# Kernel tuning notes

Hardware: AMD Instinct MI355X
Metric: run time of the kernel (lower is better)

The kernel has to match this reference:

```python
import math
import jax, jax.numpy as jnp
import numpy as np

B, S, D = 2, 2048, 4096
H = 32
HD = D // H  # 128
CLIP_QKV = 8.0
ALIBI_BIAS_MAX = 8
LN_EPS = 1e-5


def _get_alibi_slopes(total_num_heads: int, alibi_bias_max: int) -> np.ndarray:
    next_pow2 = 2 ** math.ceil(math.log2(total_num_heads))
    m = np.arange(1, next_pow2 + 1, dtype=np.float32) * (alibi_bias_max / next_pow2)
    slopes = 1.0 / np.power(2.0, m)
    if next_pow2 != total_num_heads:
        slopes = np.concatenate([slopes[1::2], slopes[::2]])[:total_num_heads]
    return slopes


ALIBI_SLOPES = jnp.asarray(_get_alibi_slopes(H, ALIBI_BIAS_MAX))  # [H]


def _layernorm(x, w, b):
    mu = jnp.mean(x, axis=-1, keepdims=True)
    var = jnp.mean(jnp.square(x - mu), axis=-1, keepdims=True)
    return (x - mu) * jax.lax.rsqrt(var + LN_EPS) * w + b


def setup_inputs() -> dict:
    key = jax.random.key(0)
    ks = jax.random.split(key, 3)
    scale_in = 1.0 / math.sqrt(D)
    return {
        "hidden_states": jax.random.normal(ks[0], (B, S, D), jnp.float32),
        "Wqkv": jax.random.normal(ks[1], (D, 3 * D), jnp.float32) * scale_in,
        "Wout": jax.random.normal(ks[2], (D, D), jnp.float32) * scale_in,
        "q_ln_w": jnp.ones((D,), jnp.float32),
        "q_ln_b": jnp.zeros((D,), jnp.float32),
        "k_ln_w": jnp.ones((D,), jnp.float32),
        "k_ln_b": jnp.zeros((D,), jnp.float32),
    }


def reference(hidden_states, Wqkv, Wout, q_ln_w, q_ln_b, k_ln_w, k_ln_b):
    # QKV projection + clamp
    qkv = jnp.clip(hidden_states @ Wqkv, -CLIP_QKV, CLIP_QKV)  # [B,S,3D]
    q, k, v = jnp.split(qkv, [D, 2 * D], axis=-1)
    # QK LayerNorm over full d_model (as in MPT qk_ln)
    q = _layernorm(q, q_ln_w, q_ln_b)
    k = _layernorm(k, k_ln_w, k_ln_b)
    # split heads
    q = q.reshape(B, S, H, HD)
    k = k.reshape(B, S, H, HD)
    v = v.reshape(B, S, H, HD)
    scale = HD ** (-0.5)
    scores = jnp.einsum("bqhd,bkhd->bhqk", q, k) * scale  # [B,H,S,S]
    # ALiBi bias: -slope * (i - j), causal mask j <= i
    pos = jnp.arange(S)
    dist = pos[:, None] - pos[None, :]  # [S,S], i - j
    bias = -ALIBI_SLOPES[:, None, None] * dist.astype(jnp.float32)  # [H,S,S]
    causal = dist >= 0
    scores = jnp.where(causal[None, None], scores + bias[None], -jnp.inf)
    attn = jax.nn.softmax(scores, axis=-1)
    out = jnp.einsum("bhqk,bkhd->bqhd", attn, v).reshape(B, S, D)
    return out @ Wout
```

## Files before the change

kernel.cpp:

```cpp
#include <hip/hip_runtime.h>
#include <hip/hip_bf16.h>
#include <stdint.h>

#define BB 2
#define SS 2048
#define DD 4096
#define HH 32
#define HDD 128

typedef unsigned short u16;
typedef unsigned int u32;

constexpr float CLIPV  = 8.0f;
constexpr float LN_EPS_ = 1e-5f;
constexpr float SCALE_ = 0.08838834764831845f;
constexpr float LOG2E_ = 1.4426950408889634f;

using f32x4 = __attribute__((ext_vector_type(4))) float;
using s16x8 = __attribute__((ext_vector_type(8))) short;

__device__ inline u16 f2bf(float f) {
  union { float f; u32 u; } v; v.f = f;
  u32 r = (v.u + 0x7FFFu + ((v.u >> 16) & 1u)) >> 16;
  return (u16)r;
}
__device__ inline float bf2f(u16 u) {
  union { u32 u; float f; } v; v.u = ((u32)u) << 16;
  return v.f;
}

typedef __attribute__((address_space(1))) void gvoid;
typedef __attribute__((address_space(3))) void lvoid;
__device__ inline void gload_lds16(const void* g, void* l) {
  __builtin_amdgcn_global_load_lds((gvoid*)g, (lvoid*)l, 16, 0, 0);
}

__device__ inline f32x4 mfma16(s16x8 a, s16x8 b, f32x4 c) {
  return __builtin_amdgcn_mfma_f32_16x16x32_bf16(a, b, c, 0, 0, 0);
}

__global__ void k_cvt_bf16(const float* __restrict__ in, u16* __restrict__ out, int nvec) {
  int i = blockIdx.x * 256 + threadIdx.x;
  if (i >= nvec) return;
  float4 a = ((const float4*)in)[i * 2];
  float4 b = ((const float4*)in)[i * 2 + 1];
  u16 tmp[8];
  tmp[0] = f2bf(a.x); tmp[1] = f2bf(a.y); tmp[2] = f2bf(a.z); tmp[3] = f2bf(a.w);
  tmp[4] = f2bf(b.x); tmp[5] = f2bf(b.y); tmp[6] = f2bf(b.z); tmp[7] = f2bf(b.w);
  ((uint4*)out)[i] = *(const uint4*)tmp;
}

__global__ void k_transpose_cvt(const float* __restrict__ src, u16* __restrict__ dst, int R, int C) {
  __shared__ float tile[32][33];
  int c0 = blockIdx.x * 32, r0 = blockIdx.y * 32;
  int tx = threadIdx.x & 31, ty = threadIdx.x >> 5;
  #pragma unroll
  for (int i = 0; i < 32; i += 8)
    tile[ty + i][tx] = src[(size_t)(r0 + ty + i) * C + (c0 + tx)];
  __syncthreads();
  #pragma unroll
  for (int i = 0; i < 32; i += 8)
    dst[(size_t)(c0 + ty + i) * R + (r0 + tx)] = f2bf(tile[tx][ty + i]);
}

__device__ __forceinline__ void stage_half(u16* ldsHalf, const u16* g, int K, int tid) {
  #pragma unroll
  for (int it = 0; it < 2; ++it) {
    int p = (it << 9) + tid;
    int row = p >> 3;
    int slotk = (p & 7) ^ (row & 7);
    gload_lds16(g + (size_t)row * K + (slotk << 3), ldsHalf + ((size_t)p << 3));
  }
}

#define DSR(dst, adr, IMM) \
  asm volatile("ds_read_b128 %0, %1 offset:" #IMM : "=v"(dst) : "v"(adr) : "memory")

#define RD_B1(a0, a1)            \
  DSR(bB_[0][0], a0, 4096);      \
  DSR(bB_[0][1], a1, 4096);      \
  DSR(bB_[1][0], a0, 6144);      \
  DSR(bB_[1][1], a1, 6144);

#define RD_A1(a0, a1)            \
  DSR(aN[0][0], a0, 8192);       \
  DSR(aN[0][1], a1, 8192);       \
  DSR(aN[1][0], a0, 10240);      \
  DSR(aN[1][1], a1, 10240);      \
  DSR(aN[2][0], a0, 12288);      \
  DSR(aN[2][1], a1, 12288);      \
  DSR(aN[3][0], a0, 14336);      \
  DSR(aN[3][1], a1, 14336);

#define RD_A0(a0, a1)            \
  DSR(aC[0][0], a0, 0);          \
  DSR(aC[0][1], a1, 0);          \
  DSR(aC[1][0], a0, 2048);       \
  DSR(aC[1][1], a1, 2048);       \
  DSR(aC[2][0], a0, 4096);       \
  DSR(aC[2][1], a1, 4096);       \
  DSR(aC[3][0], a0, 6144);       \
  DSR(aC[3][1], a1, 6144);

#define RD_B0(a0, a1)            \
  DSR(bA_[0][0], a0, 0);         \
  DSR(bA_[0][1], a1, 0);         \
  DSR(bA_[1][0], a0, 2048);      \
  DSR(bA_[1][1], a1, 2048);

#define LGKM(N)                                                    \
  asm volatile("s_waitcnt lgkmcnt(" #N ")" ::: "memory");          \
  __builtin_amdgcn_sched_barrier(0);

#define MQ(AF, BF, MB, JB)                                                    \
  _Pragma("unroll")                                                           \
  for (int i_ = 0; i_ < 4; ++i_) {                                            \
    _Pragma("unroll")                                                         \
    for (int jj_ = 0; jj_ < 2; ++jj_) {                                       \
      acc[(MB) + i_][(JB) + jj_] =                                            \
          mfma16(AF[i_][0], BF[jj_][0], acc[(MB) + i_][(JB) + jj_]);          \
      acc[(MB) + i_][(JB) + jj_] =                                            \
          mfma16(AF[i_][1], BF[jj_][1], acc[(MB) + i_][(JB) + jj_]);          \
    }                                                                         \
  }

template <int EPI>
__launch_bounds__(512)
__global__ void k_gemm256(const u16* __restrict__ A, const u16* __restrict__ Bt,
                          void* __restrict__ Cout, int M, int N, int K, int nBY) {
  __shared__ u16 lds[65536];
  u16* sA = lds;
  u16* sB = lds + 32768;
  const int tid = threadIdx.x;
  const int lane = tid & 63, w = tid >> 6;
  const int wm = w >> 2, wn = w & 3;
  const int lg = lane >> 4, lc = lane & 15;

  const int nwg = gridDim.x;
  const int cpx = nwg >> 3;
  const int id2 = (blockIdx.x & 7) * cpx + (blockIdx.x >> 3);
  const int bx = id2 / nBY, by = id2 % nBY;
  const int m0 = by * 256, n0 = bx * 256;

  const int NT = K >> 6;
  const u16* gA = A  + (size_t)m0 * K;
  const u16* gB = Bt + (size_t)n0 * K;

  const int xt0 = ((lg) ^ (lc & 7)) * 8;
  const int rowoff = lc * 64;

  const u32 aBase0 = (u32)(2 * (wm * 8192 + rowoff + xt0));
  const u32 bBase0 = (u32)(2 * (32768 + (wn >> 1) * 8192 + (wn & 1) * 4096 + rowoff + xt0));

  f32x4 acc[8][4];
  #pragma unroll
  for (int i = 0; i < 8; ++i)
    #pragma unroll
    for (int j = 0; j < 4; ++j) acc[i][j] = (f32x4){0.f, 0.f, 0.f, 0.f};

  stage_half(sA,         gA,                        K, tid);
  stage_half(sA + 8192,  gA + (size_t)128 * K,      K, tid);
  stage_half(sB,         gB,                        K, tid);
  stage_half(sB + 8192,  gB + (size_t)128 * K,      K, tid);
  stage_half(sB + 16384, gB + 64,                   K, tid);
  stage_half(sB + 24576, gB + (size_t)128 * K + 64, K, tid);
  stage_half(sA + 24576, gA + (size_t)128 * K + 64, K, tid);
  asm volatile("s_waitcnt vmcnt(0)" ::: "memory");
  __builtin_amdgcn_s_barrier();

  s16x8 aC[4][2], aN[4][2], bA_[2][2], bB_[2][2];
  {
    u32 a0 = aBase0, a1 = aBase0 ^ 64;
    u32 b0 = bBase0, b1 = bBase0 ^ 64;
    RD_A0(a0, a1)
    RD_B0(b0, b1)
  }

  for (int t = 0; t < NT; ++t) {
    const int d = t & 1;
    const bool m1 = (t + 1 < NT);
    const bool m2 = (t + 2 < NT);
    const u32 dx = d ? 32768u : 0u;
    const u32 a0 = aBase0 ^ dx, a1 = a0 ^ 64;
    const u32 b0 = bBase0 ^ dx, b1 = b0 ^ 64;
    const u32 an0 = a0 ^ 32768u, an1 = a1 ^ 32768u;
    const u32 bn0 = b0 ^ 32768u, bn1 = b1 ^ 32768u;

    RD_B1(b0, b1)
    if (m1) stage_half(sA + (d ^ 1) * 16384, gA + (size_t)(t + 1) * 64, K, tid);
    LGKM(4)
    __builtin_amdgcn_s_setprio(1);
    MQ(aC, bA_, 0, 0)
    __builtin_amdgcn_s_setprio(0);
    __builtin_amdgcn_s_barrier();

    RD_A1(a0, a1)
    if (m2) stage_half(sB + d * 16384, gB + (size_t)(t + 2) * 64, K, tid);
    LGKM(8)
    __builtin_amdgcn_s_setprio(1);
    MQ(aC, bB_, 0, 2)
    __builtin_amdgcn_s_setprio(0);
    __builtin_amdgcn_s_barrier();

    if (m2) stage_half(sB + d * 16384 + 8192, gB + (size_t)128 * K + (size_t)(t + 2) * 64, K, tid);
    LGKM(0)
    __builtin_amdgcn_s_setprio(1);
    MQ(aN, bA_, 4, 0)
    __builtin_amdgcn_s_setprio(0);
    if (m2) { asm volatile("s_waitcnt vmcnt(4)" ::: "memory"); }
    else    { asm volatile("s_waitcnt vmcnt(0)" ::: "memory"); }
    __builtin_amdgcn_s_barrier();

    if (m1) {
      RD_A0(an0, an1)
      RD_B0(bn0, bn1)
      if (m2) stage_half(sA + d * 16384 + 8192, gA + (size_t)128 * K + (size_t)(t + 2) * 64, K, tid);
    }
    __builtin_amdgcn_sched_barrier(0);
    __builtin_amdgcn_s_setprio(1);
    MQ(aN, bB_, 4, 2)
    __builtin_amdgcn_s_setprio(0);
    if (m2) { asm volatile("s_waitcnt vmcnt(2)" ::: "memory"); }
    else    { asm volatile("s_waitcnt vmcnt(0)" ::: "memory"); }
    __builtin_amdgcn_s_barrier();
  }

  #pragma unroll
  for (int i = 0; i < 8; ++i)
    #pragma unroll
    for (int j = 0; j < 4; ++j)
      #pragma unroll
      for (int r = 0; r < 4; ++r) {
        int m = m0 + wm * 128 + i * 16 + lg * 4 + r;
        int n = n0 + wn * 64 + j * 16 + lc;
        float v = acc[i][j][r];
        if (EPI == 0) {
          v = fminf(fmaxf(v, -CLIPV), CLIPV);
          ((u16*)Cout)[(size_t)m * N + n] = f2bf(v);
        } else {
          ((float*)Cout)[(size_t)m * N + n] = v;
        }
      }
}

__device__ inline void unpack8(uint4 u, float* f) {
  const u16* p = (const u16*)&u;
  #pragma unroll
  for (int j = 0; j < 8; ++j) f[j] = bf2f(p[j]);
}

__global__ void k_ln_reorder(const u16* __restrict__ qkv,
                             const float* __restrict__ qw, const float* __restrict__ qb,
                             const float* __restrict__ kw, const float* __restrict__ kb,
                             u16* __restrict__ Qo, u16* __restrict__ Ko) {
  const int row = blockIdx.x;
  const int b = row >> 11, s = row & 2047;
  const int t = threadIdx.x;
  const int lane = t & 63, w = t >> 6;
  const uint4* base = (const uint4*)(qkv + (size_t)row * (3 * DD));

  __shared__ float redsum[8], redss[8];

  uint4 q4[2], k4[2];
  q4[0] = base[t];        q4[1] = base[256 + t];
  k4[0] = base[512 + t];  k4[1] = base[768 + t];

  float qx[16], kx[16];
  unpack8(q4[0], qx); unpack8(q4[1], qx + 8);
  unpack8(k4[0], kx); unpack8(k4[1], kx + 8);

  float qs = 0.f, qss = 0.f, ks = 0.f, kss = 0.f;
  #pragma unroll
  for (int i = 0; i < 16; ++i) {
    qs += qx[i]; qss += qx[i] * qx[i];
    ks += kx[i]; kss += kx[i] * kx[i];
  }
  #pragma unroll
  for (int off = 1; off < 64; off <<= 1) {
    qs  += __shfl_xor(qs, off);  qss += __shfl_xor(qss, off);
    ks  += __shfl_xor(ks, off);  kss += __shfl_xor(kss, off);
  }
  if (lane == 0) { redsum[w] = qs; redss[w] = qss; redsum[4 + w] = ks; redss[4 + w] = kss; }
  __syncthreads();
  float qsum = redsum[0] + redsum[1] + redsum[2] + redsum[3];
  float qs2  = redss[0]  + redss[1]  + redss[2]  + redss[3];
  float ksum = redsum[4] + redsum[5] + redsum[6] + redsum[7];
  float ks2  = redss[4]  + redss[5]  + redss[6]  + redss[7];
  const float inv = 1.0f / (float)DD;
  float qmu = qsum * inv, qvar = qs2 * inv - qmu * qmu;
  float kmu = ksum * inv, kvar = ks2 * inv - kmu * kmu;
  float qrs = rsqrtf(qvar + LN_EPS_);
  float krs = rsqrtf(kvar + LN_EPS_);

  #pragma unroll
  for (int ch = 0; ch < 2; ++ch) {
    int c0 = ch * 2048 + t * 8;
    int hh = c0 >> 7, hd0 = c0 & 127;
    size_t idx = (((size_t)b * HH + hh) * SS + s) * HDD + hd0;
    {
      float4 w0 = *(const float4*)(qw + c0), w1 = *(const float4*)(qw + c0 + 4);
      float4 b0 = *(const float4*)(qb + c0), b1 = *(const float4*)(qb + c0 + 4);
      float wa[8] = {w0.x, w0.y, w0.z, w0.w, w1.x, w1.y, w1.z, w1.w};
      float ba[8] = {b0.x, b0.y, b0.z, b0.w, b1.x, b1.y, b1.z, b1.w};
      u16 tmp[8];
      #pragma unroll
      for (int j = 0; j < 8; ++j)
        tmp[j] = f2bf((qx[ch * 8 + j] - qmu) * qrs * wa[j] + ba[j]);
      *(uint4*)(Qo + idx) = *(const uint4*)tmp;
    }
    {
      float4 w0 = *(const float4*)(kw + c0), w1 = *(const float4*)(kw + c0 + 4);
      float4 b0 = *(const float4*)(kb + c0), b1 = *(const float4*)(kb + c0 + 4);
      float wa[8] = {w0.x, w0.y, w0.z, w0.w, w1.x, w1.y, w1.z, w1.w};
      float ba[8] = {b0.x, b0.y, b0.z, b0.w, b1.x, b1.y, b1.z, b1.w};
      u16 tmp[8];
      #pragma unroll
      for (int j = 0; j < 8; ++j)
        tmp[j] = f2bf((kx[ch * 8 + j] - kmu) * krs * wa[j] + ba[j]);
      *(uint4*)(Ko + idx) = *(const uint4*)tmp;
    }
  }
}

__global__ void k_transpose_v(const u16* __restrict__ qkv, u16* __restrict__ Vt) {
  __shared__ u16 ls[64 * 65];
  const int s0 = blockIdx.x * 64;
  const int hd0 = blockIdx.y * 64;
  const int bh = blockIdx.z;
  const int b = bh >> 5, h = bh & 31;
  const int t = threadIdx.x;
  const u16* src = qkv + (size_t)(b * SS + s0) * (3 * DD) + 2 * DD + h * HDD + hd0;
  #pragma unroll
  for (int it = 0; it < 4; ++it) {
    int idx = it * 256 + t;
    int sr = idx >> 4, hc = idx & 15;
    uint2 v = *(const uint2*)(src + (size_t)sr * (3 * DD) + hc * 4);
    const u16* pv = (const u16*)&v;
    #pragma unroll
    for (int j = 0; j < 4; ++j) ls[sr * 65 + hc * 4 + j] = pv[j];
  }
  __syncthreads();
  u16* dst = Vt + ((size_t)bh * HDD + hd0) * SS + s0;
  #pragma unroll
  for (int it = 0; it < 4; ++it) {
    int idx = it * 256 + t;
    int hd = idx >> 4, sc = idx & 15;
    u16 tmp[4];
    #pragma unroll
    for (int j = 0; j < 4; ++j) tmp[j] = ls[(4 * sc + j) * 65 + hd];
    *(uint2*)(dst + (size_t)hd * SS + 4 * sc) = *(const uint2*)tmp;
  }
}

__global__ __launch_bounds__(512)
void k_attn(const u16* __restrict__ Qg, const u16* __restrict__ Kg,
            const u16* __restrict__ Vt, u16* __restrict__ Og) {
  const int bid = blockIdx.x;
  const int id2 = ((bid & 7) << 7) + (bid >> 3);
  const int bh = id2 >> 4;
  const int qt = id2 & 15;
  const int b = bh >> 5, h = bh & 31;
  const int t = threadIdx.x;
  const int lane = t & 63, w = t >> 6;
  const int lg = lane >> 4, lc = lane & 15;
  const float slope = exp2f(-0.25f * (float)(h + 1));

  __shared__ u16 lK[2][8192];
  __shared__ u16 lV[2][8192];
  __shared__ u16 lP[8][1024];

  const int q0 = qt * 128 + w * 16;
  const size_t bhS = (size_t)bh * SS;
  const u16* Kbase = Kg + bhS * HDD;
  const u16* Vbase = Vt + bhS * HDD;

  s16x8 qf[4];
  {
    const u16* qrow = Qg + (bhS + q0 + lc) * HDD;
    #pragma unroll
    for (int kt = 0; kt < 4; ++kt) qf[kt] = *(const s16x8*)(qrow + kt * 32 + lg * 8);
  }

  f32x4 ot[8];
  #pragma unroll
  for (int hf = 0; hf < 8; ++hf) ot[hf] = (f32x4){0.f, 0.f, 0.f, 0.f};
  float m_r = -1e30f, l_r = 0.f;

  #define STAGE_KV(D, KV0)                                                         \
    {                                                                              \
      _Pragma("unroll")                                                            \
      for (int it_ = 0; it_ < 2; ++it_) {                                          \
        int sl = it_ * 512 + t;                                                    \
        int row = sl >> 4, k16 = sl & 15;                                          \
        gload_lds16(Kbase + (size_t)((KV0) + row) * HDD + ((k16 ^ (row & 7)) * 8), \
                    &lK[D][sl * 8]);                                               \
      }                                                                            \
      _Pragma("unroll")                                                            \
      for (int it_ = 0; it_ < 2; ++it_) {                                          \
        int sl = it_ * 512 + t;                                                    \
        int row = sl >> 3, k8 = sl & 7;                                            \
        gload_lds16(Vbase + (size_t)row * SS + (KV0) + ((k8 ^ (row & 7)) * 8),     \
                    &lV[D][sl * 8]);                                               \
      }                                                                            \
    }

  STAGE_KV(0, 0)
  __syncthreads();

  const int nt = 2 * qt + 2;
  for (int itn = 0; itn < nt; ++itn) {
    const int d = itn & 1;
    const int kv0 = itn * 64;
    if (itn + 1 < nt) STAGE_KV(d ^ 1, kv0 + 64)

    if (kv0 <= q0 + 15) {
      f32x4 st[4];
      #pragma unroll
      for (int i = 0; i < 4; ++i) {
        st[i] = (f32x4){0.f, 0.f, 0.f, 0.f};
        #pragma unroll
        for (int kt = 0; kt < 4; ++kt) {
          int r = i * 16 + lc;
          const s16x8 ka = *(const s16x8*)&lK[d][r * 128 + (((kt * 4 + lg) ^ (r & 7)) * 8)];
          st[i] = mfma16(ka, qf[kt], st[i]);
        }
      }

      float sc[4][4];
      float pm = -1e30f;
      const int qg = q0 + lc;
      #pragma unroll
      for (int i = 0; i < 4; ++i)
        #pragma unroll
        for (int r = 0; r < 4; ++r) {
          int kv = kv0 + i * 16 + lg * 4 + r;
          float x = (kv <= qg) ? st[i][r] * SCALE_ - slope * (float)(qg - kv) : -1e30f;
          sc[i][r] = x;
          pm = fmaxf(pm, x);
        }
      pm = fmaxf(pm, __shfl_xor(pm, 16));
      pm = fmaxf(pm, __shfl_xor(pm, 32));
      float m_new = fmaxf(m_r, pm);
      float alpha = exp2f((m_r - m_new) * LOG2E_);
      float rsum = 0.f;
      #pragma unroll
      for (int i = 0; i < 4; ++i) {
        float p0 = exp2f((sc[i][0] - m_new) * LOG2E_);
        float p1 = exp2f((sc[i][1] - m_new) * LOG2E_);
        float p2 = exp2f((sc[i][2] - m_new) * LOG2E_);
        float p3 = exp2f((sc[i][3] - m_new) * LOG2E_);
        rsum += (p0 + p1) + (p2 + p3);
        u32 dlo, dhi;
        asm("v_cvt_pk_bf16_f32 %0, %1, %2" : "=v"(dlo) : "v"(p0), "v"(p1));
        asm("v_cvt_pk_bf16_f32 %0, %1, %2" : "=v"(dhi) : "v"(p2), "v"(p3));
        int addr = lc * 64 + (((4 * i + lg) ^ (2 * (lc & 7))) * 4);
        uint2 val; val.x = dlo; val.y = dhi;
        *(uint2*)&lP[w][addr] = val;
      }
      rsum += __shfl_xor(rsum, 16);
      rsum += __shfl_xor(rsum, 32);
      l_r = l_r * alpha + rsum;
      m_r = m_new;

      #pragma unroll
      for (int hf = 0; hf < 8; ++hf) {
        ot[hf][0] *= alpha; ot[hf][1] *= alpha; ot[hf][2] *= alpha; ot[hf][3] *= alpha;
      }

      #pragma unroll
      for (int ks = 0; ks < 2; ++ks) {
        const int m = 4 * ks + lg;
        const s16x8 pa = *(const s16x8*)&lP[w][lc * 64 + ((m ^ (lc & 7)) * 8)];
        #pragma unroll
        for (int hf = 0; hf < 8; ++hf) {
          int row = hf * 16 + lc;
          const s16x8 vb = *(const s16x8*)&lV[d][row * 64 + ((m ^ (row & 7)) * 8)];
          ot[hf] = mfma16(vb, pa, ot[hf]);
        }
      }
    }
    __syncthreads();
  }
  #undef STAGE_KV

  float linv = 1.f / l_r;
  const size_t obase = ((size_t)(b * SS + q0 + lc)) * DD + h * HDD;
  #pragma unroll
  for (int hf = 0; hf < 8; ++hf) {
    u16 tmp[4];
    #pragma unroll
    for (int r = 0; r < 4; ++r) tmp[r] = f2bf(ot[hf][r] * linv);
    *(uint2*)&Og[obase + hf * 16 + lg * 4] = *(const uint2*)tmp;
  }
}

extern "C" void kernel_launch(void* const* d_in, const int* in_sizes, int n_in,
                              void* d_out, int out_size, void* d_ws, size_t ws_size,
                              hipStream_t stream) {
  const float* hidden = (const float*)d_in[0];
  const float* Wqkv   = (const float*)d_in[1];
  const float* Wout   = (const float*)d_in[2];
  const float* qw     = (const float*)d_in[3];
  const float* qb     = (const float*)d_in[4];
  const float* kw     = (const float*)d_in[5];
  const float* kb     = (const float*)d_in[6];
  float* out = (float*)d_out;
  char* ws = (char*)d_ws;

  u16* Xb    = (u16*)(ws);
  u16* WqkvT = (u16*)(ws + 33554432);
  u16* Qb    = (u16*)(ws + 33554432);
  u16* Kb    = (u16*)(ws + 67108864);
  u16* Vtb   = (u16*)(ws + 100663296);
  u16* WoutT = (u16*)(ws + 134217728);
  u16* qkv   = (u16*)(ws + 167772160);
  u16* attnO = Xb;

  k_cvt_bf16<<<8192, 256, 0, stream>>>(hidden, Xb, 2097152);
  k_transpose_cvt<<<dim3(12288 / 32, 4096 / 32), 256, 0, stream>>>(Wqkv, WqkvT, 4096, 12288);
  k_transpose_cvt<<<dim3(4096 / 32, 4096 / 32), 256, 0, stream>>>(Wout, WoutT, 4096, 4096);
  k_gemm256<0><<<768, 512, 0, stream>>>(Xb, WqkvT, qkv, 4096, 12288, 4096, 16);
  k_ln_reorder<<<4096, 256, 0, stream>>>(qkv, qw, qb, kw, kb, Qb, Kb);
  k_transpose_v<<<dim3(SS / 64, HDD / 64, BB * HH), 256, 0, stream>>>(qkv, Vtb);
  k_attn<<<1024, 512, 0, stream>>>(Qb, Kb, Vtb, attnO);
  k_gemm256<1><<<256, 512, 0, stream>>>(attnO, WoutT, out, 4096, 4096, 4096, 16);
}
```

Baseline: 798.0 us.

## Switch GEMM to 32x32 MFMA tiles and reverse attention KV order with lazy rescale

The 256x256 GEMM now uses 32x32x16 bf16 MFMA instructions with new LDS read addressing, in place of 16x16x32. This cuts the number of MFMA issues and LDS fragment reads per tile. The attention loop now walks KV tiles from the diagonal backward, which lets the running max settle early. It skips the O/l rescale when no lane's max grows, and precomputes ALiBi offsets with a fast path for fully unmasked tiles. The risks are a changed accumulator output mapping, a different register footprint, and a warp-divergent branch on the max update.

```diff
diff --git a/kernel.cpp b/kernel.cpp
--- a/kernel.cpp
+++ b/kernel.cpp
@@ -16,8 +16,9 @@
 constexpr float SCALE_ = 0.08838834764831845f;
 constexpr float LOG2E_ = 1.4426950408889634f;
 
-using f32x4 = __attribute__((ext_vector_type(4))) float;
-using s16x8 = __attribute__((ext_vector_type(8))) short;
+using f32x4  = __attribute__((ext_vector_type(4))) float;
+using f32x16 = __attribute__((ext_vector_type(16))) float;
+using s16x8  = __attribute__((ext_vector_type(8))) short;
 
 __device__ inline u16 f2bf(float f) {
   union { float f; u32 u; } v; v.f = f;
@@ -37,6 +38,9 @@
 
 __device__ inline f32x4 mfma16(s16x8 a, s16x8 b, f32x4 c) {
   return __builtin_amdgcn_mfma_f32_16x16x32_bf16(a, b, c, 0, 0, 0);
+}
+__device__ inline f32x16 mfma32(s16x8 a, s16x8 b, f32x16 c) {
+  return __builtin_amdgcn_mfma_f32_32x32x16_bf16(a, b, c, 0, 0, 0);
 }
 
 __global__ void k_cvt_bf16(const float* __restrict__ in, u16* __restrict__ out, int nvec) {
@@ -76,52 +80,47 @@
 #define DSR(dst, adr, IMM) \
   asm volatile("ds_read_b128 %0, %1 offset:" #IMM : "=v"(dst) : "v"(adr) : "memory")
 
-#define RD_B1(a0, a1)            \
-  DSR(bB_[0][0], a0, 4096);      \
-  DSR(bB_[0][1], a1, 4096);      \
-  DSR(bB_[1][0], a0, 6144);      \
-  DSR(bB_[1][1], a1, 6144);
-
-#define RD_A1(a0, a1)            \
-  DSR(aN[0][0], a0, 8192);       \
-  DSR(aN[0][1], a1, 8192);       \
-  DSR(aN[1][0], a0, 10240);      \
-  DSR(aN[1][1], a1, 10240);      \
-  DSR(aN[2][0], a0, 12288);      \
-  DSR(aN[2][1], a1, 12288);      \
-  DSR(aN[3][0], a0, 14336);      \
-  DSR(aN[3][1], a1, 14336);
-
-#define RD_A0(a0, a1)            \
-  DSR(aC[0][0], a0, 0);          \
-  DSR(aC[0][1], a1, 0);          \
-  DSR(aC[1][0], a0, 2048);       \
-  DSR(aC[1][1], a1, 2048);       \
-  DSR(aC[2][0], a0, 4096);       \
-  DSR(aC[2][1], a1, 4096);       \
-  DSR(aC[3][0], a0, 6144);       \
-  DSR(aC[3][1], a1, 6144);
-
-#define RD_B0(a0, a1)            \
-  DSR(bA_[0][0], a0, 0);         \
-  DSR(bA_[0][1], a1, 0);         \
-  DSR(bA_[1][0], a0, 2048);      \
-  DSR(bA_[1][1], a1, 2048);
+#define RD_A01(k0, k1, k2, k3)       \
+  DSR(aC[0][0], k0, 0);              \
+  DSR(aC[0][1], k1, 0);              \
+  DSR(aC[0][2], k2, 0);              \
+  DSR(aC[0][3], k3, 0);              \
+  DSR(aC[1][0], k0, 4096);           \
+  DSR(aC[1][1], k1, 4096);           \
+  DSR(aC[1][2], k2, 4096);           \
+  DSR(aC[1][3], k3, 4096);
+
+#define RD_A23(k0, k1, k2, k3)       \
+  DSR(aN[0][0], k0, 8192);           \
+  DSR(aN[0][1], k1, 8192);           \
+  DSR(aN[0][2], k2, 8192);           \
+  DSR(aN[0][3], k3, 8192);           \
+  DSR(aN[1][0], k0, 12288);          \
+  DSR(aN[1][1], k1, 12288);          \
+  DSR(aN[1][2], k2, 12288);          \
+  DSR(aN[1][3], k3, 12288);
+
+#define RD_BN0(k0, k1, k2, k3)       \
+  DSR(bA_[0], k0, 0);                \
+  DSR(bA_[1], k1, 0);                \
+  DSR(bA_[2], k2, 0);                \
+  DSR(bA_[3], k3, 0);
+
+#define RD_BN1(k0, k1, k2, k3)       \
+  DSR(bB_[0], k0, 4096);             \
+  DSR(bB_[1], k1, 4096);             \
+  DSR(bB_[2], k2, 4096);             \
+  DSR(bB_[3], k3, 4096);
 
 #define LGKM(N)                                                    \
   asm volatile("s_waitcnt lgkmcnt(" #N ")" ::: "memory");          \
   __builtin_amdgcn_sched_barrier(0);
 
-#define MQ(AF, BF, MB, JB)                                                    \
+#define MQ32(AF, BF, MB, NT)                                                  \
   _Pragma("unroll")                                                           \
-  for (int i_ = 0; i_ < 4; ++i_) {                                            \
-    _Pragma("unroll")                                                         \
-    for (int jj_ = 0; jj_ < 2; ++jj_) {                                       \
-      acc[(MB) + i_][(JB) + jj_] =                                            \
-          mfma16(AF[i_][0], BF[jj_][0], acc[(MB) + i_][(JB) + jj_]);          \
-      acc[(MB) + i_][(JB) + jj_] =                                            \
-          mfma16(AF[i_][1], BF[jj_][1], acc[(MB) + i_][(JB) + jj_]);          \
-    }                                                                         \
+  for (int kc_ = 0; kc_ < 4; ++kc_) {                                         \
+    acc[(MB)][NT]     = mfma32(AF[0][kc_], BF[kc_], acc[(MB)][NT]);           \
+    acc[(MB) + 1][NT] = mfma32(AF[1][kc_], BF[kc_], acc[(MB) + 1][NT]);       \
   }
 
 template <int EPI>
@@ -134,7 +133,7 @@
   const int tid = threadIdx.x;
   const int lane = tid & 63, w = tid >> 6;
   const int wm = w >> 2, wn = w & 3;
-  const int lg = lane >> 4, lc = lane & 15;
+  const int r31 = lane & 31, g32 = lane >> 5, e7 = lane & 7;
 
   const int nwg = gridDim.x;
   const int cpx = nwg >> 3;
@@ -146,17 +145,21 @@
   const u16* gA = A  + (size_t)m0 * K;
   const u16* gB = Bt + (size_t)n0 * K;
 
-  const int xt0 = ((lg) ^ (lc & 7)) * 8;
-  const int rowoff = lc * 64;
-
-  const u32 aBase0 = (u32)(2 * (wm * 8192 + rowoff + xt0));
-  const u32 bBase0 = (u32)(2 * (32768 + (wn >> 1) * 8192 + (wn & 1) * 4096 + rowoff + xt0));
-
-  f32x4 acc[8][4];
-  #pragma unroll
-  for (int i = 0; i < 8; ++i)
-    #pragma unroll
-    for (int j = 0; j < 4; ++j) acc[i][j] = (f32x4){0.f, 0.f, 0.f, 0.f};
+  u32 aBs[4], bBs[4];
+  #pragma unroll
+  for (int kc = 0; kc < 4; ++kc) {
+    int slot = ((kc << 1) | g32) ^ e7;
+    aBs[kc] = (u32)(wm * 16384 + r31 * 128 + slot * 16);
+    bBs[kc] = (u32)(65536 + (wn >> 1) * 16384 + (wn & 1) * 8192 + r31 * 128 + slot * 16);
+  }
+
+  f32x16 acc[4][2];
+  #pragma unroll
+  for (int i = 0; i < 4; ++i)
+    #pragma unroll
+    for (int j = 0; j < 2; ++j)
+      #pragma unroll
+      for (int r = 0; r < 16; ++r) acc[i][j][r] = 0.f;
 
   stage_half(sA,         gA,                        K, tid);
   stage_half(sA + 8192,  gA + (size_t)128 * K,      K, tid);
@@ -168,57 +171,53 @@
   asm volatile("s_waitcnt vmcnt(0)" ::: "memory");
   __builtin_amdgcn_s_barrier();
 
-  s16x8 aC[4][2], aN[4][2], bA_[2][2], bB_[2][2];
-  {
-    u32 a0 = aBase0, a1 = aBase0 ^ 64;
-    u32 b0 = bBase0, b1 = bBase0 ^ 64;
-    RD_A0(a0, a1)
-    RD_B0(b0, b1)
-  }
+  s16x8 aC[2][4], aN[2][4], bA_[4], bB_[4];
+  RD_A01(aBs[0], aBs[1], aBs[2], aBs[3])
+  RD_BN0(bBs[0], bBs[1], bBs[2], bBs[3])
 
   for (int t = 0; t < NT; ++t) {
     const int d = t & 1;
     const bool m1 = (t + 1 < NT);
     const bool m2 = (t + 2 < NT);
     const u32 dx = d ? 32768u : 0u;
-    const u32 a0 = aBase0 ^ dx, a1 = a0 ^ 64;
-    const u32 b0 = bBase0 ^ dx, b1 = b0 ^ 64;
-    const u32 an0 = a0 ^ 32768u, an1 = a1 ^ 32768u;
-    const u32 bn0 = b0 ^ 32768u, bn1 = b1 ^ 32768u;
-
-    RD_B1(b0, b1)
+    const u32 aD0 = aBs[0] ^ dx, aD1 = aBs[1] ^ dx, aD2 = aBs[2] ^ dx, aD3 = aBs[3] ^ dx;
+    const u32 bD0 = bBs[0] ^ dx, bD1 = bBs[1] ^ dx, bD2 = bBs[2] ^ dx, bD3 = bBs[3] ^ dx;
+    const u32 aX0 = aD0 ^ 32768u, aX1 = aD1 ^ 32768u, aX2 = aD2 ^ 32768u, aX3 = aD3 ^ 32768u;
+    const u32 bX0 = bD0 ^ 32768u, bX1 = bD1 ^ 32768u, bX2 = bD2 ^ 32768u, bX3 = bD3 ^ 32768u;
+
+    RD_BN1(bD0, bD1, bD2, bD3)
     if (m1) stage_half(sA + (d ^ 1) * 16384, gA + (size_t)(t + 1) * 64, K, tid);
     LGKM(4)
     __builtin_amdgcn_s_setprio(1);
-    MQ(aC, bA_, 0, 0)
+    MQ32(aC, bA_, 0, 0)
     __builtin_amdgcn_s_setprio(0);
     __builtin_amdgcn_s_barrier();
 
-    RD_A1(a0, a1)
+    RD_A23(aD0, aD1, aD2, aD3)
     if (m2) stage_half(sB + d * 16384, gB + (size_t)(t + 2) * 64, K, tid);
     LGKM(8)
     __builtin_amdgcn_s_setprio(1);
-    MQ(aC, bB_, 0, 2)
+    MQ32(aC, bB_, 0, 1)
     __builtin_amdgcn_s_setprio(0);
     __builtin_amdgcn_s_barrier();
 
     if (m2) stage_half(sB + d * 16384 + 8192, gB + (size_t)128 * K + (size_t)(t + 2) * 64, K, tid);
     LGKM(0)
     __builtin_amdgcn_s_setprio(1);
-    MQ(aN, bA_, 4, 0)
+    MQ32(aN, bA_, 2, 0)
     __builtin_amdgcn_s_setprio(0);
     if (m2) { asm volatile("s_waitcnt vmcnt(4)" ::: "memory"); }
     else    { asm volatile("s_waitcnt vmcnt(0)" ::: "memory"); }
     __builtin_amdgcn_s_barrier();
 
     if (m1) {
-      RD_A0(an0, an1)
-      RD_B0(bn0, bn1)
+      RD_A01(aX0, aX1, aX2, aX3)
+      RD_BN0(bX0, bX1, bX2, bX3)
       if (m2) stage_half(sA + d * 16384 + 8192, gA + (size_t)128 * K + (size_t)(t + 2) * 64, K, tid);
     }
     __builtin_amdgcn_sched_barrier(0);
     __builtin_amdgcn_s_setprio(1);
-    MQ(aN, bB_, 4, 2)
+    MQ32(aN, bB_, 2, 1)
     __builtin_amdgcn_s_setprio(0);
     if (m2) { asm volatile("s_waitcnt vmcnt(2)" ::: "memory"); }
     else    { asm volatile("s_waitcnt vmcnt(0)" ::: "memory"); }
@@ -226,14 +225,14 @@
   }
 
   #pragma unroll
-  for (int i = 0; i < 8; ++i)
-    #pragma unroll
-    for (int j = 0; j < 4; ++j)
-      #pragma unroll
-      for (int r = 0; r < 4; ++r) {
-        int m = m0 + wm * 128 + i * 16 + lg * 4 + r;
-        int n = n0 + wn * 64 + j * 16 + lc;
-        float v = acc[i][j][r];
+  for (int mt = 0; mt < 4; ++mt)
+    #pragma unroll
+    for (int nt = 0; nt < 2; ++nt)
+      #pragma unroll
+      for (int r = 0; r < 16; ++r) {
+        int m = m0 + wm * 128 + mt * 32 + (r & 3) + 8 * (r >> 2) + 4 * g32;
+        int n = n0 + wn * 64 + nt * 32 + r31;
+        float v = acc[mt][nt][r];
         if (EPI == 0) {
           v = fminf(fmaxf(v, -CLIPV), CLIPV);
           ((u16*)Cout)[(size_t)m * N + n] = f2bf(v);
@@ -381,10 +380,17 @@
     for (int kt = 0; kt < 4; ++kt) qf[kt] = *(const s16x8*)(qrow + kt * 32 + lg * 8);
   }
 
+  float sKt[16];
+  #pragma unroll
+  for (int i = 0; i < 4; ++i)
+    #pragma unroll
+    for (int r = 0; r < 4; ++r) sKt[i * 4 + r] = slope * (float)(i * 16 + lg * 4 + r);
+
   f32x4 ot[8];
   #pragma unroll
   for (int hf = 0; hf < 8; ++hf) ot[hf] = (f32x4){0.f, 0.f, 0.f, 0.f};
   float m_r = -1e30f, l_r = 0.f;
+  const int qg = q0 + lc;
 
   #define STAGE_KV(D, KV0)                                                         \
     {                                                                              \
@@ -404,14 +410,14 @@
       }                                                                            \
     }
 
-  STAGE_KV(0, 0)
+  const int nt = 2 * qt + 2;
+  STAGE_KV((nt - 1) & 1, (nt - 1) * 64)
   __syncthreads();
 
-  const int nt = 2 * qt + 2;
-  for (int itn = 0; itn < nt; ++itn) {
+  for (int itn = nt - 1; itn >= 0; --itn) {
     const int d = itn & 1;
     const int kv0 = itn * 64;
-    if (itn + 1 < nt) STAGE_KV(d ^ 1, kv0 + 64)
+    if (itn > 0) STAGE_KV(d ^ 1, kv0 - 64)
 
     if (kv0 <= q0 + 15) {
       f32x4 st[4];
@@ -428,27 +434,50 @@
 
       float sc[4][4];
       float pm = -1e30f;
-      const int qg = q0 + lc;
-      #pragma unroll
-      for (int i = 0; i < 4; ++i)
+      const float c0 = slope * (float)(kv0 - qg);
+      if (kv0 + 63 <= q0) {
         #pragma unroll
-        for (int r = 0; r < 4; ++r) {
-          int kv = kv0 + i * 16 + lg * 4 + r;
-          float x = (kv <= qg) ? st[i][r] * SCALE_ - slope * (float)(qg - kv) : -1e30f;
-          sc[i][r] = x;
-          pm = fmaxf(pm, x);
-        }
+        for (int i = 0; i < 4; ++i)
+          #pragma unroll
+          for (int r = 0; r < 4; ++r) {
+            float x = fmaf(st[i][r], SCALE_, c0 + sKt[i * 4 + r]);
+            sc[i][r] = x;
+            pm = fmaxf(pm, x);
+          }
+      } else {
+        const int thr2 = (qg - kv0) - lg * 4;
+        #pragma unroll
+        for (int i = 0; i < 4; ++i)
+          #pragma unroll
+          for (int r = 0; r < 4; ++r) {
+            float x = ((i * 16 + r) <= thr2)
+                          ? fmaf(st[i][r], SCALE_, c0 + sKt[i * 4 + r])
+                          : -1e30f;
+            sc[i][r] = x;
+            pm = fmaxf(pm, x);
+          }
+      }
       pm = fmaxf(pm, __shfl_xor(pm, 16));
       pm = fmaxf(pm, __shfl_xor(pm, 32));
-      float m_new = fmaxf(m_r, pm);
-      float alpha = exp2f((m_r - m_new) * LOG2E_);
+
+      if (__any(pm > m_r)) {
+        float m_new = fmaxf(m_r, pm);
+        float alpha = exp2f((m_r - m_new) * LOG2E_);
+        #pragma unroll
+        for (int hf = 0; hf < 8; ++hf) {
+          ot[hf][0] *= alpha; ot[hf][1] *= alpha; ot[hf][2] *= alpha; ot[hf][3] *= alpha;
+        }
+        l_r *= alpha;
+        m_r = m_new;
+      }
+
       float rsum = 0.f;
       #pragma unroll
       for (int i = 0; i < 4; ++i) {
-        float p0 = exp2f((sc[i][0] - m_new) * LOG2E_);
-        float p1 = exp2f((sc[i][1] - m_new) * LOG2E_);
-        float p2 = exp2f((sc[i][2] - m_new) * LOG2E_);
-        float p3 = exp2f((sc[i][3] - m_new) * LOG2E_);
+        float p0 = exp2f((sc[i][0] - m_r) * LOG2E_);
+        float p1 = exp2f((sc[i][1] - m_r) * LOG2E_);
+        float p2 = exp2f((sc[i][2] - m_r) * LOG2E_);
+        float p3 = exp2f((sc[i][3] - m_r) * LOG2E_);
         rsum += (p0 + p1) + (p2 + p3);
         u32 dlo, dhi;
         asm("v_cvt_pk_bf16_f32 %0, %1, %2" : "=v"(dlo) : "v"(p0), "v"(p1));
@@ -459,13 +488,7 @@
       }
       rsum += __shfl_xor(rsum, 16);
       rsum += __shfl_xor(rsum, 32);
-      l_r = l_r * alpha + rsum;
-      m_r = m_new;
-
-      #pragma unroll
-      for (int hf = 0; hf < 8; ++hf) {
-        ot[hf][0] *= alpha; ot[hf][1] *= alpha; ot[hf][2] *= alpha; ot[hf][3] *= alpha;
-      }
+      l_r += rsum;
 
       #pragma unroll
       for (int ks = 0; ks < 2; ++ks) {
```

After: 1.184 ms. 48.4% more time.
